# Performance work log

Measured on AMD Instinct MI355X. Metric: run time of the kernel, lower is better.

Reference implementation:

```python
import jax, jax.numpy as jnp
import numpy as np
from jax import lax

B, H, W = 64, 64, 64
N_CHANNELS = 16
N_FILTERS = 128
N_DENSE = 256
T_STEPS = 60  # update_time() with Tmin=60, Tmax=61


def setup_inputs() -> dict:
    key = jax.random.key(0)
    ks = jax.random.split(key, 7)
    s_conv = 1.0 / np.sqrt(3 * 3 * N_CHANNELS)
    s_d1 = 1.0 / np.sqrt(N_FILTERS)
    s_d2 = 1.0 / np.sqrt(N_DENSE)
    return {
        "input": jax.random.uniform(ks[0], (B, H, W), dtype=jnp.float32),
        # conv kernel in HWIO layout for lax.conv_general_dilated
        "conv_w": jax.random.uniform(ks[1], (3, 3, N_CHANNELS, N_FILTERS), jnp.float32, -s_conv, s_conv),
        "conv_b": jax.random.uniform(ks[2], (N_FILTERS,), jnp.float32, -s_conv, s_conv),
        "w1": jax.random.uniform(ks[3], (N_FILTERS, N_DENSE), jnp.float32, -s_d1, s_d1),
        "b1": jax.random.uniform(ks[4], (N_DENSE,), jnp.float32, -s_d1, s_d1),
        "w2": jax.random.uniform(ks[5], (N_DENSE, N_CHANNELS), jnp.float32, -s_d2, s_d2),
        "b2": jax.random.uniform(ks[6], (N_CHANNELS,), jnp.float32, -s_d2, s_d2),
    }


def reference(input, conv_w, conv_b, w1, b1, w2, b2):
    # grid: (B,H,W,C), channel 0 seeded with the input image
    grid = jnp.zeros((B, H, W, N_CHANNELS), dtype=input.dtype)
    grid = grid.at[..., 0].set(input)
    # zero channel 0 of the delta (channel 0 is frozen)
    ch_mask = (jnp.arange(N_CHANNELS) != 0).astype(input.dtype)  # (C,)

    def step(g, _):
        conv = lax.conv_general_dilated(
            g, conv_w, window_strides=(1, 1), padding="SAME",
            dimension_numbers=("NHWC", "HWIO", "NHWC")) + conv_b
        h = jax.nn.relu(conv)                       # (B,H,W,F)
        d = jax.nn.relu(h @ w1 + b1) @ w2 + b2      # (B,H,W,C)
        alive = (g[..., 0:1] > 0.1).astype(g.dtype)  # (B,H,W,1)
        g = g + d * ch_mask * alive
        return g, None

    grid, _ = lax.scan(step, grid, None, length=T_STEPS)
    return jax.nn.softmax(grid[..., 1:11], axis=-1)  # (B,H,W,10)
```

## Files before the change

kernel.cpp:

```cpp
#include <hip/hip_runtime.h>
#include <math.h>

typedef _Float16 f16;
typedef f16  f16x8 __attribute__((ext_vector_type(8)));
typedef f16  f16x4 __attribute__((ext_vector_type(4)));
typedef float f32x4 __attribute__((ext_vector_type(4)));

#define NB 64
#define NC 16
#define NF 128
#define ND 256
#define NSTEP 60
#define GRID_ELEMS (NB*64*64*NC)
#define NPIX (NB*64*64)

#define KCONV 160
#define HSS   136
#define RPS   18
#define ASS   72

#define OFF_CW 0
#define OFF_W1 20480
#define OFF_W2 53248

__global__ void init_grid(const float* __restrict__ inp, float* __restrict__ g) {
    int i = blockIdx.x * 256 + threadIdx.x;
    if (i >= GRID_ELEMS) return;
    int c = i & 15;
    g[i] = (c == 0) ? inp[i >> 4] : 0.0f;
}

__global__ void prep_weights(const float* __restrict__ cw, const float* __restrict__ w1,
                             const float* __restrict__ w2, f16* __restrict__ wb) {
    int i = blockIdx.x * 256 + threadIdx.x;
    float v; int off, idx;
    if (i < 20480) {
        int f = i / 160, k = i - f * 160;
        v = (k < 144) ? cw[k * 128 + f] : 0.0f;
        off = OFF_CW; idx = i;
    } else if (i < 20480 + 32768) {
        int r = i - 20480;
        int j = r >> 7, f = r & 127;
        v = w1[f * 256 + j];
        off = OFF_W1; idx = r;
    } else {
        int r = i - 20480 - 32768;
        int c = r >> 8, j = r & 255;
        v = w2[j * 16 + c];
        off = OFF_W2; idx = r;
    }
    wb[off + idx] = (f16)v;
}

__global__ __launch_bounds__(256, 2) void nca_step(
    const float* __restrict__ gin, float* __restrict__ gout,
    const f16* __restrict__ wb,
    const float* __restrict__ cb, const float* __restrict__ b1, const float* __restrict__ b2)
{
    __shared__ f16 smem[40000];
    f16* const hs   = smem;
    f16* const un   = smem + 34816;
    f16* const halo = un;
    f16* const aScr = un;
    float* const redF = (float*)smem;

    const int t    = threadIdx.x;
    const int w    = t >> 6;
    const int lane = t & 63;
    const int q    = lane >> 4;
    const int l16  = lane & 15;

    const int d  = blockIdx.x;
    const int b  = ((d & 7) << 3) | (d >> 7);
    const int tl = (d >> 3) & 15;
    const int y0 = (tl >> 2) << 4;
    const int x0 = (tl & 3) << 4;

    const float* gb  = gin  + (size_t)b * 64 * 64 * 16;
    float*       gob = gout + (size_t)b * 64 * 64 * 16;

    const int fbase = w << 5;
    f16x8 cA[2][5];
    #pragma unroll
    for (int ft = 0; ft < 2; ++ft)
        #pragma unroll
        for (int kc = 0; kc < 5; ++kc)
            cA[ft][kc] = *(const f16x8*)(wb + OFF_CW +
                (size_t)(fbase + ft * 16 + l16) * KCONV + kc * 32 + q * 8);
    const int jbase = w << 6;
    f16x8 w2f[2];
    #pragma unroll
    for (int jp = 0; jp < 2; ++jp)
        w2f[jp] = *(const f16x8*)(wb + OFF_W2 + (size_t)l16 * 256 + jbase + jp * 32 + q * 8);

    for (int i = t; i < 1296; i += 256) {
        int c4 = (i & 3) << 2;
        int xy = i >> 2;
        int xx = xy % 18;
        int yy = xy / 18;
        int gy = y0 + yy - 1, gx = x0 + xx - 1;
        f32x4 v = {0.f, 0.f, 0.f, 0.f};
        if ((unsigned)gy < 64u && (unsigned)gx < 64u)
            v = *(const f32x4*)(gb + (gy * 64 + gx) * 16 + c4);
        f16x4 hv;
        hv.x = (f16)v.x; hv.y = (f16)v.y; hv.z = (f16)v.z; hv.w = (f16)v.w;
        *(f16x4*)(halo + xy * 16 + c4) = hv;
    }
    __syncthreads();

    for (int half = 0; half < 2; ++half) {
        f32x4 acc[2][8];
        #pragma unroll
        for (int ft = 0; ft < 2; ++ft) {
            f32x4 bias;
            bias.x = cb[fbase + ft * 16 + q * 4 + 0];
            bias.y = cb[fbase + ft * 16 + q * 4 + 1];
            bias.z = cb[fbase + ft * 16 + q * 4 + 2];
            bias.w = cb[fbase + ft * 16 + q * 4 + 3];
            #pragma unroll
            for (int p = 0; p < 8; ++p) acc[ft][p] = bias;
        }

        #pragma unroll
        for (int kc = 0; kc < 5; ++kc) {
            int tap = kc * 2 + (q >> 1);
            if (tap > 8) tap = 8;
            int dy = tap / 3, dx = tap - dy * 3;
            #pragma unroll
            for (int p = 0; p < 8; ++p) {
                int hy = half * 8 + p + dy;
                int hx = l16 + dx;
                f16x8 bf = *(const f16x8*)(halo + (hy * 18 + hx) * 16 + (q & 1) * 8);
                #pragma unroll
                for (int ft = 0; ft < 2; ++ft)
                    acc[ft][p] = __builtin_amdgcn_mfma_f32_16x16x32_f16(cA[ft][kc], bf, acc[ft][p], 0, 0, 0);
            }
        }

        #pragma unroll
        for (int ft = 0; ft < 2; ++ft)
            #pragma unroll
            for (int p = 0; p < 8; ++p) {
                f32x4 a = acc[ft][p];
                f16x4 pk;
                pk.x = (f16)fmaxf(a.x, 0.0f);
                pk.y = (f16)fmaxf(a.y, 0.0f);
                pk.z = (f16)fmaxf(a.z, 0.0f);
                pk.w = (f16)fmaxf(a.w, 0.0f);
                *(f16x4*)(hs + (half * 128 + p * 16 + l16) * HSS + fbase + ft * 16 + q * 4) = pk;
            }
    }
    __syncthreads();

    f16x8 dA[2][2][4];
    float b1v[2][2][4];
    #pragma unroll
    for (int jp = 0; jp < 2; ++jp)
        #pragma unroll
        for (int jt2 = 0; jt2 < 2; ++jt2) {
            #pragma unroll
            for (int kc = 0; kc < 4; ++kc)
                dA[jp][jt2][kc] = *(const f16x8*)(wb + OFF_W1 +
                    (size_t)(jbase + jp * 32 + jt2 * 16 + l16) * 128 + kc * 32 + q * 8);
            #pragma unroll
            for (int r = 0; r < 4; ++r)
                b1v[jp][jt2][r] = b1[jbase + jp * 32 + jt2 * 16 + q * 4 + r];
        }

    f32x4 dacc[16];
    #pragma unroll
    for (int p = 0; p < 16; ++p) { dacc[p].x = 0.f; dacc[p].y = 0.f; dacc[p].z = 0.f; dacc[p].w = 0.f; }

    f16* const myScr = aScr + (w * 16 + l16) * ASS;

    for (int p = 0; p < 16; ++p) {
        f16x8 hB[4];
        #pragma unroll
        for (int kc = 0; kc < 4; ++kc)
            hB[kc] = *(const f16x8*)(hs + (p * 16 + l16) * HSS + kc * 32 + q * 8);

        #pragma unroll
        for (int jp = 0; jp < 2; ++jp)
            #pragma unroll
            for (int jt2 = 0; jt2 < 2; ++jt2) {
                f32x4 a1;
                a1.x = b1v[jp][jt2][0]; a1.y = b1v[jp][jt2][1];
                a1.z = b1v[jp][jt2][2]; a1.w = b1v[jp][jt2][3];
                #pragma unroll
                for (int kc = 0; kc < 4; ++kc)
                    a1 = __builtin_amdgcn_mfma_f32_16x16x32_f16(dA[jp][jt2][kc], hB[kc], a1, 0, 0, 0);
                f16x4 pk;
                pk.x = (f16)fmaxf(a1.x, 0.0f);
                pk.y = (f16)fmaxf(a1.y, 0.0f);
                pk.z = (f16)fmaxf(a1.z, 0.0f);
                pk.w = (f16)fmaxf(a1.w, 0.0f);
                *(f16x4*)(myScr + jp * 32 + jt2 * 16 + q * 4) = pk;
            }
        f16x8 af0 = *(const f16x8*)(myScr + q * 8);
        f16x8 af1 = *(const f16x8*)(myScr + 32 + q * 8);
        dacc[p] = __builtin_amdgcn_mfma_f32_16x16x32_f16(af0, w2f[0], dacc[p], 0, 0, 0);
        dacc[p] = __builtin_amdgcn_mfma_f32_16x16x32_f16(af1, w2f[1], dacc[p], 0, 0, 0);
    }

    __syncthreads();
    #pragma unroll
    for (int p = 0; p < 16; ++p)
        #pragma unroll
        for (int r = 0; r < 4; ++r) {
            int px = p * 16 + q * 4 + r;
            redF[(w * 256 + px) * RPS + l16] = dacc[p][r];
        }
    __syncthreads();

    {
        const int px = t;
        const int yy = px >> 4, xx = px & 15;
        const size_t pixb = ((size_t)(y0 + yy) * 64 + (x0 + xx)) * 16;
        const float a0 = gb[pixb];
        const bool alive = (a0 > 0.1f);
        #pragma unroll
        for (int h = 0; h < 4; ++h) {
            const int ch = h * 4;
            f32x4 v0 = *(const f32x4*)(redF + (0 * 256 + px) * RPS + ch);
            f32x4 v1 = *(const f32x4*)(redF + (1 * 256 + px) * RPS + ch);
            f32x4 v2 = *(const f32x4*)(redF + (2 * 256 + px) * RPS + ch);
            f32x4 v3 = *(const f32x4*)(redF + (3 * 256 + px) * RPS + ch);
            f32x4 sv = v0 + v1 + v2 + v3;
            f32x4 gv = *(const f32x4*)(gb + pixb + ch);
            f32x4 ov;
            #pragma unroll
            for (int i = 0; i < 4; ++i) {
                int c = ch + i;
                float nv = gv[i];
                if (alive && c != 0) nv += sv[i] + b2[c];
                ov[i] = nv;
            }
            *(f32x4*)(gob + pixb + ch) = ov;
        }
    }
}

__global__ void softmax_out(const float* __restrict__ g, float* __restrict__ out) {
    int pix = blockIdx.x * 256 + threadIdx.x;
    if (pix >= NPIX) return;
    const float* gp = g + (size_t)pix * 16;
    float v[10];
    float m = -1e30f;
    #pragma unroll
    for (int i = 0; i < 10; ++i) { v[i] = gp[1 + i]; m = fmaxf(m, v[i]); }
    float s = 0.f;
    #pragma unroll
    for (int i = 0; i < 10; ++i) { v[i] = __expf(v[i] - m); s += v[i]; }
    float inv = 1.0f / s;
    float* op = out + (size_t)pix * 10;
    #pragma unroll
    for (int i = 0; i < 10; ++i) op[i] = v[i] * inv;
}

extern "C" void kernel_launch(void* const* d_in, const int* in_sizes, int n_in,
                              void* d_out, int out_size, void* d_ws, size_t ws_size,
                              hipStream_t stream) {
    const float* inp = (const float*)d_in[0];
    const float* cw  = (const float*)d_in[1];
    const float* cb  = (const float*)d_in[2];
    const float* w1  = (const float*)d_in[3];
    const float* b1  = (const float*)d_in[4];
    const float* w2  = (const float*)d_in[5];
    const float* b2  = (const float*)d_in[6];
    float* out = (float*)d_out;

    float* g0 = (float*)d_ws;
    float* g1 = g0 + GRID_ELEMS;
    f16* wb = (f16*)d_out;

    prep_weights<<<224, 256, 0, stream>>>(cw, w1, w2, wb);
    init_grid<<<(GRID_ELEMS + 255) / 256, 256, 0, stream>>>(inp, g0);

    float* bufs[2] = { g0, g1 };
    for (int s = 0; s < NSTEP; ++s) {
        nca_step<<<1024, 256, 0, stream>>>(bufs[s & 1], bufs[(s + 1) & 1],
                                           wb, cb, b1, b2);
    }
    softmax_out<<<(NPIX + 255) / 256, 256, 0, stream>>>(g0, out);
}
```

Baseline: 2.566 ms.

## Halve step tile to 8x16, chain dense layers in registers, raise occupancy

```diff
diff --git a/kernel.cpp b/kernel.cpp
--- a/kernel.cpp
+++ b/kernel.cpp
@@ -17,7 +17,6 @@
 #define KCONV 160
 #define HSS   136
 #define RPS   18
-#define ASS   72
 
 #define OFF_CW 0
 #define OFF_W1 20480
@@ -52,16 +51,14 @@
     wb[off + idx] = (f16)v;
 }
 
-__global__ __launch_bounds__(256, 2) void nca_step(
+__global__ __launch_bounds__(256, 3) void nca_step(
     const float* __restrict__ gin, float* __restrict__ gout,
     const f16* __restrict__ wb,
     const float* __restrict__ cb, const float* __restrict__ b1, const float* __restrict__ b2)
 {
-    __shared__ f16 smem[40000];
+    __shared__ f16 smem[21312];
     f16* const hs   = smem;
-    f16* const un   = smem + 34816;
-    f16* const halo = un;
-    f16* const aScr = un;
+    f16* const halo = smem + 18432;
     float* const redF = (float*)smem;
 
     const int t    = threadIdx.x;
@@ -71,9 +68,10 @@
     const int l16  = lane & 15;
 
     const int d  = blockIdx.x;
-    const int b  = ((d & 7) << 3) | (d >> 7);
-    const int tl = (d >> 3) & 15;
-    const int y0 = (tl >> 2) << 4;
+    const int kk = d >> 3;
+    const int b  = ((d & 7) << 3) | (kk >> 5);
+    const int tl = kk & 31;
+    const int y0 = (tl >> 2) << 3;
     const int x0 = (tl & 3) << 4;
 
     const float* gb  = gin  + (size_t)b * 64 * 64 * 16;
@@ -87,13 +85,8 @@
         for (int kc = 0; kc < 5; ++kc)
             cA[ft][kc] = *(const f16x8*)(wb + OFF_CW +
                 (size_t)(fbase + ft * 16 + l16) * KCONV + kc * 32 + q * 8);
-    const int jbase = w << 6;
-    f16x8 w2f[2];
-    #pragma unroll
-    for (int jp = 0; jp < 2; ++jp)
-        w2f[jp] = *(const f16x8*)(wb + OFF_W2 + (size_t)l16 * 256 + jbase + jp * 32 + q * 8);
-
-    for (int i = t; i < 1296; i += 256) {
+
+    for (int i = t; i < 720; i += 256) {
         int c4 = (i & 3) << 2;
         int xy = i >> 2;
         int xx = xy % 18;
@@ -108,7 +101,7 @@
     }
     __syncthreads();
 
-    for (int half = 0; half < 2; ++half) {
+    {
         f32x4 acc[2][8];
         #pragma unroll
         for (int ft = 0; ft < 2; ++ft) {
@@ -128,7 +121,7 @@
             int dy = tap / 3, dx = tap - dy * 3;
             #pragma unroll
             for (int p = 0; p < 8; ++p) {
-                int hy = half * 8 + p + dy;
+                int hy = p + dy;
                 int hx = l16 + dx;
                 f16x8 bf = *(const f16x8*)(halo + (hy * 18 + hx) * 16 + (q & 1) * 8);
                 #pragma unroll
@@ -147,11 +140,12 @@
                 pk.y = (f16)fmaxf(a.y, 0.0f);
                 pk.z = (f16)fmaxf(a.z, 0.0f);
                 pk.w = (f16)fmaxf(a.w, 0.0f);
-                *(f16x4*)(hs + (half * 128 + p * 16 + l16) * HSS + fbase + ft * 16 + q * 4) = pk;
-            }
-    }
-    __syncthreads();
-
+                *(f16x4*)(hs + (p * 16 + l16) * HSS + fbase + ft * 16 + q * 4) = pk;
+            }
+    }
+    __syncthreads();
+
+    const int jbase = w << 6;
     f16x8 dA[2][2][4];
     float b1v[2][2][4];
     #pragma unroll
@@ -166,14 +160,16 @@
             for (int r = 0; r < 4; ++r)
                 b1v[jp][jt2][r] = b1[jbase + jp * 32 + jt2 * 16 + q * 4 + r];
         }
-
-    f32x4 dacc[16];
-    #pragma unroll
-    for (int p = 0; p < 16; ++p) { dacc[p].x = 0.f; dacc[p].y = 0.f; dacc[p].z = 0.f; dacc[p].w = 0.f; }
-
-    f16* const myScr = aScr + (w * 16 + l16) * ASS;
-
-    for (int p = 0; p < 16; ++p) {
+    f16x4 w2k[4];
+    #pragma unroll
+    for (int jt = 0; jt < 4; ++jt)
+        w2k[jt] = *(const f16x4*)(wb + OFF_W2 + (size_t)l16 * 256 + jbase + jt * 16 + q * 4);
+
+    f32x4 dacc[8];
+    #pragma unroll
+    for (int p = 0; p < 8; ++p) { dacc[p].x = 0.f; dacc[p].y = 0.f; dacc[p].z = 0.f; dacc[p].w = 0.f; }
+
+    for (int p = 0; p < 8; ++p) {
         f16x8 hB[4];
         #pragma unroll
         for (int kc = 0; kc < 4; ++kc)
@@ -194,37 +190,34 @@
                 pk.y = (f16)fmaxf(a1.y, 0.0f);
                 pk.z = (f16)fmaxf(a1.z, 0.0f);
                 pk.w = (f16)fmaxf(a1.w, 0.0f);
-                *(f16x4*)(myScr + jp * 32 + jt2 * 16 + q * 4) = pk;
-            }
-        f16x8 af0 = *(const f16x8*)(myScr + q * 8);
-        f16x8 af1 = *(const f16x8*)(myScr + 32 + q * 8);
-        dacc[p] = __builtin_amdgcn_mfma_f32_16x16x32_f16(af0, w2f[0], dacc[p], 0, 0, 0);
-        dacc[p] = __builtin_amdgcn_mfma_f32_16x16x32_f16(af1, w2f[1], dacc[p], 0, 0, 0);
-    }
-
-    __syncthreads();
-    #pragma unroll
-    for (int p = 0; p < 16; ++p)
+                dacc[p] = __builtin_amdgcn_mfma_f32_16x16x16f16(pk, w2k[jp * 2 + jt2], dacc[p], 0, 0, 0);
+            }
+    }
+
+    __syncthreads();
+    #pragma unroll
+    for (int p = 0; p < 8; ++p)
         #pragma unroll
         for (int r = 0; r < 4; ++r) {
             int px = p * 16 + q * 4 + r;
-            redF[(w * 256 + px) * RPS + l16] = dacc[p][r];
+            redF[(w * 128 + px) * RPS + l16] = dacc[p][r];
         }
     __syncthreads();
 
     {
-        const int px = t;
+        const int px  = t >> 1;
+        const int ch0 = (t & 1) << 3;
         const int yy = px >> 4, xx = px & 15;
         const size_t pixb = ((size_t)(y0 + yy) * 64 + (x0 + xx)) * 16;
         const float a0 = gb[pixb];
         const bool alive = (a0 > 0.1f);
         #pragma unroll
-        for (int h = 0; h < 4; ++h) {
-            const int ch = h * 4;
-            f32x4 v0 = *(const f32x4*)(redF + (0 * 256 + px) * RPS + ch);
-            f32x4 v1 = *(const f32x4*)(redF + (1 * 256 + px) * RPS + ch);
-            f32x4 v2 = *(const f32x4*)(redF + (2 * 256 + px) * RPS + ch);
-            f32x4 v3 = *(const f32x4*)(redF + (3 * 256 + px) * RPS + ch);
+        for (int h = 0; h < 2; ++h) {
+            const int ch = ch0 + h * 4;
+            f32x4 v0 = *(const f32x4*)(redF + (0 * 128 + px) * RPS + ch);
+            f32x4 v1 = *(const f32x4*)(redF + (1 * 128 + px) * RPS + ch);
+            f32x4 v2 = *(const f32x4*)(redF + (2 * 128 + px) * RPS + ch);
+            f32x4 v3 = *(const f32x4*)(redF + (3 * 128 + px) * RPS + ch);
             f32x4 sv = v0 + v1 + v2 + v3;
             f32x4 gv = *(const f32x4*)(gb + pixb + ch);
             f32x4 ov;
@@ -278,7 +271,7 @@
 
     float* bufs[2] = { g0, g1 };
     for (int s = 0; s < NSTEP; ++s) {
-        nca_step<<<1024, 256, 0, stream>>>(bufs[s & 1], bufs[(s + 1) & 1],
+        nca_step<<<2048, 256, 0, stream>>>(bufs[s & 1], bufs[(s + 1) & 1],
                                            wb, cb, b1, b2);
     }
     softmax_out<<<(NPIX + 255) / 256, 256, 0, stream>>>(g0, out);
```

New measurement: 2.695 ms. 1.05x slower.
